# Optimization experiments

Measured on AMD Instinct MI355X. Metric: run time of the kernel, lower is better.

The kernel has to match this reference:

```python
import jax, jax.numpy as jnp
import numpy as np

EPS = 1e-8


def setup_inputs() -> dict:
    key = jax.random.key(0)
    k1, k2, k3 = jax.random.split(key, 3)
    B, K, L, D = 4, 64, 128, 768
    context = jax.random.normal(k1, (B, K, 2, L, D), dtype=jnp.float32)
    # MlpModule(input_size=D): Linear(D, D) -> ReLU -> Linear(D, 1)
    w1 = jax.random.normal(k2, (D, D), dtype=jnp.float32) * (1.0 / np.sqrt(D))
    b1 = jnp.zeros((D,), dtype=jnp.float32)
    w2 = jax.random.normal(k3, (D, 1), dtype=jnp.float32) * (1.0 / np.sqrt(D))
    b2 = jnp.zeros((1,), dtype=jnp.float32)
    return {"context": context, "w1": w1, "b1": b1, "w2": w2, "b2": b2}


def reference(context, w1, b1, w2, b2):
    # context: [B, K, 2, L, D]; slice 0 = context tokens, slice 1 = entity tokens
    ctx = context[:, :, 0, :, :]   # [B, K, L, D]
    ent = context[:, :, 1, :, :]   # [B, K, L, D]

    ctx_norm = jnp.linalg.norm(ctx, axis=-1, keepdims=True)  # [B, K, L, 1]
    ent_norm = jnp.linalg.norm(ent, axis=-1, keepdims=True)  # [B, K, L, 1]

    # cosine-similarity score matrix: [B, K, L, L]
    denom = ctx_norm * jnp.swapaxes(ent_norm, -1, -2) + EPS
    scores = jnp.einsum('bkld,bkmd->bklm', ctx, ent) / denom

    # normalized embeddings (torch code does in-place /= before the stack)
    ctx_n = ctx / ctx_norm
    ent_n = ent / ent_norm

    # top-1 match along entity axis, gather matched entity token per context token
    argmax_idx = jnp.argmax(scores, axis=-1)                       # [B, K, L] int
    matched = jnp.take_along_axis(ent_n, argmax_idx[..., None], axis=2)  # [B, K, L, D]

    pair = jnp.stack([ctx_n, matched], axis=-2)  # [B, K, L, 2, D]

    # MLP: Linear(D,D) -> ReLU -> Linear(D,1), then sum over the pair axis
    h = jax.nn.relu(jnp.einsum('bklpd,de->bklpe', pair, w1) + b1)
    out = jnp.einsum('bklpd,do->bklpo', h, w2) + b2   # [B, K, L, 2, 1]
    out = jnp.sum(out, axis=-2)                        # [B, K, L, 1]
    return jnp.squeeze(out, axis=-1)                   # [B, K, L]
```

## Files before the change

### kernel.cpp

```cpp
#include <hip/hip_runtime.h>
#include <hip/hip_bf16.h>
#include <stdint.h>

#define NB 4
#define NK 64
#define NL 128
#define ND 768
#define NBK (NB*NK)
#define NROW (NBK*NL)
#define LD2 (NL*ND)
#define EPSF 1e-8f

typedef __bf16 bf16x8 __attribute__((ext_vector_type(8)));
typedef float  f32x4  __attribute__((ext_vector_type(4)));

__device__ __forceinline__ int row_off(int r) {
  if (r < NROW) return r*ND + (r >> 7)*LD2;
  int r2 = r - NROW;
  return r2*ND + (r2 >> 7)*LD2 + LD2;
}

__global__ __launch_bounds__(256) void k0_w1t(const float* __restrict__ w1,
                                              __bf16* __restrict__ w1t) {
  __shared__ float tile[64][68];
  int kb = (blockIdx.x / 12) * 64, eb = (blockIdx.x % 12) * 64;
  int t = threadIdx.x;
  int r = t >> 2, c0 = (t & 3) * 16;
  #pragma unroll
  for (int j = 0; j < 4; j++) {
    f32x4 v = *(const f32x4*)(w1 + (kb + r)*ND + eb + c0 + j*4);
    *(f32x4*)&tile[r][c0 + j*4] = v;
  }
  __syncthreads();
  int e = t & 63, gi = t >> 6;
  int eg = eb + e;
  #pragma unroll
  for (int g2 = 0; g2 < 2; g2++) {
    int g = gi*2 + g2;
    bf16x8 o;
    #pragma unroll
    for (int j = 0; j < 8; j++) o[j] = (__bf16)tile[g*8 + j][e];
    int G = (kb >> 3) + (g ^ (eg & 7));
    *(bf16x8*)(w1t + eg*ND + G*8) = o;
  }
}

__global__ __launch_bounds__(256) void k2_scores(
    const float* __restrict__ ctxall, float* __restrict__ norm,
    int* __restrict__ amax) {
  __shared__ float at[2][16][68];
  __shared__ float bt[2][16][132];
  __shared__ float red[256];
  __shared__ float cnorm[64], enorm[128];
  int bk = blockIdx.x >> 1, half = blockIdx.x & 1;
  const float* cbase = ctxall + bk*2*LD2 + half*64*ND;
  const float* ebase = ctxall + bk*2*LD2 + LD2;
  int tid = threadIdx.x;
  int tr = tid >> 5, tc = tid & 31;
  int ar = tid >> 2, ak = (tid & 3)*4;
  int br = tid >> 1, bkk = (tid & 1)*8;

  float acc[8][4];
  #pragma unroll
  for (int j = 0; j < 8; j++)
    #pragma unroll
    for (int c = 0; c < 4; c++) acc[j][c] = 0.f;
  float sqa = 0.f, sqb = 0.f;

  f32x4 av  = *(const f32x4*)(cbase + ar*ND + ak);
  f32x4 bv0 = *(const f32x4*)(ebase + br*ND + bkk);
  f32x4 bv1 = *(const f32x4*)(ebase + br*ND + bkk + 4);

  int p = 0;
  for (int t = 0; t < 48; t++) {
    #pragma unroll
    for (int j = 0; j < 4; j++) { at[p][ak+j][ar] = av[j];     sqa += av[j]*av[j]; }
    #pragma unroll
    for (int j = 0; j < 4; j++) { bt[p][bkk+j][br] = bv0[j];   sqb += bv0[j]*bv0[j]; }
    #pragma unroll
    for (int j = 0; j < 4; j++) { bt[p][bkk+4+j][br] = bv1[j]; sqb += bv1[j]*bv1[j]; }
    __syncthreads();
    if (t < 47) {
      int k0 = (t+1)*16;
      av  = *(const f32x4*)(cbase + ar*ND + k0 + ak);
      bv0 = *(const f32x4*)(ebase + br*ND + k0 + bkk);
      bv1 = *(const f32x4*)(ebase + br*ND + k0 + bkk + 4);
    }
    #pragma unroll
    for (int kk = 0; kk < 16; kk++) {
      f32x4 a0 = *(const f32x4*)&at[p][kk][tr*8];
      f32x4 a1 = *(const f32x4*)&at[p][kk][tr*8 + 4];
      f32x4 b  = *(const f32x4*)&bt[p][kk][tc*4];
      #pragma unroll
      for (int j = 0; j < 4; j++)
        #pragma unroll
        for (int c = 0; c < 4; c++) {
          acc[j][c]   = fmaf(a0[j], b[c], acc[j][c]);
          acc[j+4][c] = fmaf(a1[j], b[c], acc[j+4][c]);
        }
    }
    p ^= 1;
  }

  red[tid] = sqa; __syncthreads();
  if (tid < 64) {
    float s = red[tid*4] + red[tid*4+1] + red[tid*4+2] + red[tid*4+3];
    float n = sqrtf(s);
    cnorm[tid] = n;
    norm[bk*NL + half*64 + tid] = n;
  }
  __syncthreads();
  red[tid] = sqb; __syncthreads();
  if (tid < 128) {
    float s = red[tid*2] + red[tid*2+1];
    float n = sqrtf(s);
    enorm[tid] = n;
    if (half == 0) norm[NROW + bk*NL + tid] = n;
  }
  __syncthreads();

  float en[4];
  #pragma unroll
  for (int c = 0; c < 4; c++) en[c] = enorm[tc*4 + c];

  float bestv[8]; int besti[8];
  #pragma unroll
  for (int j = 0; j < 8; j++) {
    float cn = cnorm[tr*8 + j];
    bestv[j] = -3.0e38f; besti[j] = 0;
    #pragma unroll
    for (int c = 0; c < 4; c++) {
      float s = acc[j][c] / (cn*en[c] + EPSF);
      if (s > bestv[j]) { bestv[j] = s; besti[j] = tc*4 + c; }
    }
  }
  #pragma unroll
  for (int off = 1; off < 32; off <<= 1) {
    #pragma unroll
    for (int j = 0; j < 8; j++) {
      float ov = __shfl_xor(bestv[j], off);
      int   oi = __shfl_xor(besti[j], off);
      if (ov > bestv[j] || (ov == bestv[j] && oi < besti[j])) { bestv[j] = ov; besti[j] = oi; }
    }
  }
  if (tc == 0) {
    #pragma unroll
    for (int j = 0; j < 8; j++) amax[bk*NL + half*64 + tr*8 + j] = besti[j];
  }
}

__global__ __launch_bounds__(256, 2) void k3_mlp(
    const float* __restrict__ ctxall, const float* __restrict__ norm,
    const __bf16* __restrict__ w1t, const float* __restrict__ b1,
    const float* __restrict__ w2, float* __restrict__ val) {
  __shared__ alignas(16) __bf16 btile[16*768];
  int tid = threadIdx.x;
  int wave = tid >> 6, lane = tid & 63;
  int quad = lane >> 4, eloc = lane & 15;
  int rbase = blockIdx.x*128 + wave*32;

  bf16x8 afrag[2][24];
  #pragma unroll
  for (int s = 0; s < 2; s++) {
    int r = rbase + s*16 + eloc;
    const float* src = ctxall + row_off(r);
    float rinv = 1.0f / norm[r];
    #pragma unroll
    for (int ks = 0; ks < 24; ks++) {
      const float* sp = src + ks*32 + quad*8;
      f32x4 v0 = *(const f32x4*)sp;
      f32x4 v1 = *(const f32x4*)(sp + 4);
      bf16x8 a;
      a[0] = (__bf16)(v0[0]*rinv); a[1] = (__bf16)(v0[1]*rinv);
      a[2] = (__bf16)(v0[2]*rinv); a[3] = (__bf16)(v0[3]*rinv);
      a[4] = (__bf16)(v1[0]*rinv); a[5] = (__bf16)(v1[1]*rinv);
      a[6] = (__bf16)(v1[2]*rinv); a[7] = (__bf16)(v1[3]*rinv);
      afrag[s][ks] = a;
    }
  }

  float oacc[2][4] = {{0,0,0,0},{0,0,0,0}};
  for (int nt = 0; nt < 48; nt++) {
    const __bf16* gsrc = w1t + nt*16*ND;
    __syncthreads();
    #pragma unroll
    for (int i = 0; i < 6; i++) {
      __builtin_amdgcn_global_load_lds(
        (const __attribute__((address_space(1))) unsigned int*)(gsrc + (i*256 + tid)*8),
        (__attribute__((address_space(3))) unsigned int*)(btile + (i*256 + tid)*8),
        16, 0, 0);
    }
    __syncthreads();

    f32x4 h0 = {0,0,0,0}, h1 = {0,0,0,0};
    #pragma unroll
    for (int ks = 0; ks < 24; ks++) {
      int g = ks*4 + quad;
      bf16x8 bfrag = *(const bf16x8*)(btile + eloc*ND + ((g ^ (eloc & 7))*8));
      h0 = __builtin_amdgcn_mfma_f32_16x16x32_bf16(afrag[0][ks], bfrag, h0, 0, 0, 0);
      h1 = __builtin_amdgcn_mfma_f32_16x16x32_bf16(afrag[1][ks], bfrag, h1, 0, 0, 0);
    }
    float b1v = b1[nt*16 + eloc];
    float w2v = w2[nt*16 + eloc];
    #pragma unroll
    for (int rr = 0; rr < 4; rr++) {
      oacc[0][rr] += fmaxf(h0[rr] + b1v, 0.f) * w2v;
      oacc[1][rr] += fmaxf(h1[rr] + b1v, 0.f) * w2v;
    }
  }
  #pragma unroll
  for (int m = 1; m < 16; m <<= 1)
    #pragma unroll
    for (int s = 0; s < 2; s++)
      #pragma unroll
      for (int rr = 0; rr < 4; rr++)
        oacc[s][rr] += __shfl_xor(oacc[s][rr], m);
  if (eloc == 0) {
    #pragma unroll
    for (int s = 0; s < 2; s++)
      #pragma unroll
      for (int rr = 0; rr < 4; rr++)
        val[rbase + s*16 + quad*4 + rr] = oacc[s][rr];
  }
}

__global__ void k4_out(const float* __restrict__ val, const int* __restrict__ amax,
                       const float* __restrict__ b2, float* __restrict__ out) {
  int i = blockIdx.x*256 + threadIdx.x;
  int bk = i >> 7;
  out[i] = val[i] + val[NROW + bk*NL + amax[i]] + 2.0f*b2[0];
}

extern "C" void kernel_launch(void* const* d_in, const int* in_sizes, int n_in,
                              void* d_out, int out_size, void* d_ws, size_t ws_size,
                              hipStream_t stream) {
  const float* ctxall = (const float*)d_in[0];
  const float* w1 = (const float*)d_in[1];
  const float* b1 = (const float*)d_in[2];
  const float* w2 = (const float*)d_in[3];
  const float* b2 = (const float*)d_in[4];
  float* out = (float*)d_out;

  char* ws = (char*)d_ws;
  float* norm = (float*)ws;
  int*   amax = (int*)(ws + 262144);
  float* val  = (float*)(ws + 262144 + 131072);
  __bf16* w1t = (__bf16*)(ws + 655360);

  hipLaunchKernelGGL(k0_w1t,   dim3(144),         dim3(256), 0, stream, w1, w1t);
  hipLaunchKernelGGL(k2_scores,dim3(2*NBK),       dim3(256), 0, stream, ctxall, norm, amax);
  hipLaunchKernelGGL(k3_mlp,   dim3(2*NROW/128),  dim3(256), 0, stream, ctxall, norm, w1t, b1, w2, val);
  hipLaunchKernelGGL(k4_out,   dim3(NROW/256),    dim3(256), 0, stream, val, amax, b2, out);
}
```

Before: 424.2 us.

## Screen argmax with split-bf16 MFMA, rescore near-ties in fp32, double-buffer W1 tiles

```diff
diff --git a/kernel.cpp b/kernel.cpp
--- a/kernel.cpp
+++ b/kernel.cpp
@@ -10,6 +10,8 @@
 #define NROW (NBK*NL)
 #define LD2 (NL*ND)
 #define EPSF 1e-8f
+#define THETA 2e-3f
+#define CAP 16384
 
 typedef __bf16 bf16x8 __attribute__((ext_vector_type(8)));
 typedef float  f32x4  __attribute__((ext_vector_type(4)));
@@ -21,8 +23,13 @@
 }
 
 __global__ __launch_bounds__(256) void k0_w1t(const float* __restrict__ w1,
-                                              __bf16* __restrict__ w1t) {
+                                              __bf16* __restrict__ w1t,
+                                              unsigned long long* __restrict__ amax2,
+                                              unsigned* __restrict__ cntg) {
   __shared__ float tile[64][68];
+  int idx = blockIdx.x*256 + threadIdx.x;
+  if (idx < NROW) amax2[idx] = 0ull;
+  if (idx == 0) *cntg = 0u;
   int kb = (blockIdx.x / 12) * 64, eb = (blockIdx.x % 12) * 64;
   int t = threadIdx.x;
   int r = t >> 2, c0 = (t & 3) * 16;
@@ -45,107 +52,146 @@
   }
 }
 
-__global__ __launch_bounds__(256) void k2_scores(
+__device__ __forceinline__ void cvt4(f32x4 v, unsigned& hp0, unsigned& hp1,
+                                     unsigned& lp0, unsigned& lp1, float& sq) {
+  unsigned u0 = __float_as_uint(v[0]), u1 = __float_as_uint(v[1]);
+  unsigned u2 = __float_as_uint(v[2]), u3 = __float_as_uint(v[3]);
+  hp0 = (u1 & 0xffff0000u) | (u0 >> 16);
+  hp1 = (u3 & 0xffff0000u) | (u2 >> 16);
+  float l0 = v[0] - __uint_as_float(u0 & 0xffff0000u);
+  float l1 = v[1] - __uint_as_float(u1 & 0xffff0000u);
+  float l2 = v[2] - __uint_as_float(u2 & 0xffff0000u);
+  float l3 = v[3] - __uint_as_float(u3 & 0xffff0000u);
+  lp0 = (__float_as_uint(l1) & 0xffff0000u) | (__float_as_uint(l0) >> 16);
+  lp1 = (__float_as_uint(l3) & 0xffff0000u) | (__float_as_uint(l2) >> 16);
+  sq += v[0]*v[0] + v[1]*v[1] + v[2]*v[2] + v[3]*v[3];
+}
+
+__global__ __launch_bounds__(512) void k2a_screen(
     const float* __restrict__ ctxall, float* __restrict__ norm,
-    int* __restrict__ amax) {
-  __shared__ float at[2][16][68];
-  __shared__ float bt[2][16][132];
-  __shared__ float red[256];
-  __shared__ float cnorm[64], enorm[128];
-  int bk = blockIdx.x >> 1, half = blockIdx.x & 1;
-  const float* cbase = ctxall + bk*2*LD2 + half*64*ND;
-  const float* ebase = ctxall + bk*2*LD2 + LD2;
-  int tid = threadIdx.x;
-  int tr = tid >> 5, tc = tid & 31;
-  int ar = tid >> 2, ak = (tid & 3)*4;
-  int br = tid >> 1, bkk = (tid & 1)*8;
-
-  float acc[8][4];
-  #pragma unroll
-  for (int j = 0; j < 8; j++)
-    #pragma unroll
-    for (int c = 0; c < 4; c++) acc[j][c] = 0.f;
-  float sqa = 0.f, sqb = 0.f;
-
-  f32x4 av  = *(const f32x4*)(cbase + ar*ND + ak);
-  f32x4 bv0 = *(const f32x4*)(ebase + br*ND + bkk);
-  f32x4 bv1 = *(const f32x4*)(ebase + br*ND + bkk + 4);
+    int* __restrict__ amax, unsigned* __restrict__ cntg,
+    unsigned* __restrict__ list) {
+  __shared__ alignas(16) __bf16 tiles[2][4][128*32];
+  __shared__ float einv_s[128];
+  int bk = blockIdx.x;
+  int t = threadIdx.x;
+  int mat = t >> 8, row = (t >> 1) & 127, kh = (t & 1) * 16;
+  const float* src = ctxall + bk*2*LD2 + mat*LD2 + row*ND + kh;
+  int w = t >> 6, lane = t & 63, quad = lane >> 4, eloc = lane & 15;
+
+  f32x4 pv[4];
+  #pragma unroll
+  for (int i = 0; i < 4; i++) pv[i] = *(const f32x4*)(src + i*4);
+  float sq = 0.f;
+  f32x4 acc[8];
+  #pragma unroll
+  for (int ct = 0; ct < 8; ct++) acc[ct] = (f32x4){0,0,0,0};
 
   int p = 0;
-  for (int t = 0; t < 48; t++) {
-    #pragma unroll
-    for (int j = 0; j < 4; j++) { at[p][ak+j][ar] = av[j];     sqa += av[j]*av[j]; }
-    #pragma unroll
-    for (int j = 0; j < 4; j++) { bt[p][bkk+j][br] = bv0[j];   sqb += bv0[j]*bv0[j]; }
-    #pragma unroll
-    for (int j = 0; j < 4; j++) { bt[p][bkk+4+j][br] = bv1[j]; sqb += bv1[j]*bv1[j]; }
+  for (int kt = 0; kt < 24; kt++) {
+    unsigned h0,h1,h2,h3, l0,l1,l2,l3;
+    cvt4(pv[0], h0, h1, l0, l1, sq);
+    cvt4(pv[1], h2, h3, l2, l3, sq);
+    __bf16* hdst = &tiles[p][2*mat  ][row*32 + kh];
+    __bf16* ldst = &tiles[p][2*mat+1][row*32 + kh];
+    *(uint4*)hdst = make_uint4(h0,h1,h2,h3);
+    *(uint4*)ldst = make_uint4(l0,l1,l2,l3);
+    cvt4(pv[2], h0, h1, l0, l1, sq);
+    cvt4(pv[3], h2, h3, l2, l3, sq);
+    *((uint4*)hdst + 1) = make_uint4(h0,h1,h2,h3);
+    *((uint4*)ldst + 1) = make_uint4(l0,l1,l2,l3);
     __syncthreads();
-    if (t < 47) {
-      int k0 = (t+1)*16;
-      av  = *(const f32x4*)(cbase + ar*ND + k0 + ak);
-      bv0 = *(const f32x4*)(ebase + br*ND + k0 + bkk);
-      bv1 = *(const f32x4*)(ebase + br*ND + k0 + bkk + 4);
-    }
-    #pragma unroll
-    for (int kk = 0; kk < 16; kk++) {
-      f32x4 a0 = *(const f32x4*)&at[p][kk][tr*8];
-      f32x4 a1 = *(const f32x4*)&at[p][kk][tr*8 + 4];
-      f32x4 b  = *(const f32x4*)&bt[p][kk][tc*4];
-      #pragma unroll
-      for (int j = 0; j < 4; j++)
-        #pragma unroll
-        for (int c = 0; c < 4; c++) {
-          acc[j][c]   = fmaf(a0[j], b[c], acc[j][c]);
-          acc[j+4][c] = fmaf(a1[j], b[c], acc[j+4][c]);
+    if (kt < 23) {
+      const float* s2 = src + (kt+1)*32;
+      #pragma unroll
+      for (int i = 0; i < 4; i++) pv[i] = *(const f32x4*)(s2 + i*4);
+    }
+    bf16x8 ah = *(const bf16x8*)&tiles[p][0][(w*16+eloc)*32 + quad*8];
+    bf16x8 al = *(const bf16x8*)&tiles[p][1][(w*16+eloc)*32 + quad*8];
+    #pragma unroll
+    for (int ct = 0; ct < 8; ct++) {
+      bf16x8 bh = *(const bf16x8*)&tiles[p][2][(ct*16+eloc)*32 + quad*8];
+      bf16x8 bl = *(const bf16x8*)&tiles[p][3][(ct*16+eloc)*32 + quad*8];
+      acc[ct] = __builtin_amdgcn_mfma_f32_16x16x32_bf16(al, bh, acc[ct], 0, 0, 0);
+      acc[ct] = __builtin_amdgcn_mfma_f32_16x16x32_bf16(ah, bl, acc[ct], 0, 0, 0);
+      acc[ct] = __builtin_amdgcn_mfma_f32_16x16x32_bf16(ah, bh, acc[ct], 0, 0, 0);
+    }
+    p ^= 1;
+  }
+
+  float stot = sq + __shfl_xor(sq, 1);
+  if ((t & 1) == 0) {
+    float n = sqrtf(stot);
+    if (mat == 0) norm[bk*NL + row] = n;
+    else { norm[NROW + bk*NL + row] = n; einv_s[row] = 1.0f / n; }
+  }
+  __syncthreads();
+
+  #pragma unroll
+  for (int rr = 0; rr < 4; rr++) {
+    float sc[8];
+    float best = -3.0e38f; int bcol = 0;
+    #pragma unroll
+    for (int ct = 0; ct < 8; ct++) {
+      sc[ct] = acc[ct][rr] * einv_s[ct*16 + eloc];
+      int col = ct*16 + eloc;
+      if (sc[ct] > best) { best = sc[ct]; bcol = col; }
+    }
+    #pragma unroll
+    for (int m = 1; m < 16; m <<= 1) {
+      float ov = __shfl_xor(best, m);
+      int   oc = __shfl_xor(bcol, m);
+      if (ov > best || (ov == best && oc < bcol)) { best = ov; bcol = oc; }
+    }
+    int grow = bk*NL + w*16 + quad*4 + rr;
+    if (eloc == 0) amax[grow] = bcol;
+    int cnt = 0;
+    #pragma unroll
+    for (int ct = 0; ct < 8; ct++) cnt += (sc[ct] >= best - THETA) ? 1 : 0;
+    #pragma unroll
+    for (int m = 1; m < 16; m <<= 1) cnt += __shfl_xor(cnt, m);
+    if (cnt >= 2) {
+      #pragma unroll
+      for (int ct = 0; ct < 8; ct++) {
+        if (sc[ct] >= best - THETA) {
+          unsigned idx = atomicAdd(cntg, 1u);
+          if (idx < CAP) list[idx] = ((unsigned)grow << 7) | (unsigned)(ct*16 + eloc);
         }
-    }
-    p ^= 1;
-  }
-
-  red[tid] = sqa; __syncthreads();
-  if (tid < 64) {
-    float s = red[tid*4] + red[tid*4+1] + red[tid*4+2] + red[tid*4+3];
-    float n = sqrtf(s);
-    cnorm[tid] = n;
-    norm[bk*NL + half*64 + tid] = n;
-  }
-  __syncthreads();
-  red[tid] = sqb; __syncthreads();
-  if (tid < 128) {
-    float s = red[tid*2] + red[tid*2+1];
-    float n = sqrtf(s);
-    enorm[tid] = n;
-    if (half == 0) norm[NROW + bk*NL + tid] = n;
-  }
-  __syncthreads();
-
-  float en[4];
-  #pragma unroll
-  for (int c = 0; c < 4; c++) en[c] = enorm[tc*4 + c];
-
-  float bestv[8]; int besti[8];
-  #pragma unroll
-  for (int j = 0; j < 8; j++) {
-    float cn = cnorm[tr*8 + j];
-    bestv[j] = -3.0e38f; besti[j] = 0;
-    #pragma unroll
-    for (int c = 0; c < 4; c++) {
-      float s = acc[j][c] / (cn*en[c] + EPSF);
-      if (s > bestv[j]) { bestv[j] = s; besti[j] = tc*4 + c; }
-    }
-  }
-  #pragma unroll
-  for (int off = 1; off < 32; off <<= 1) {
-    #pragma unroll
-    for (int j = 0; j < 8; j++) {
-      float ov = __shfl_xor(bestv[j], off);
-      int   oi = __shfl_xor(besti[j], off);
-      if (ov > bestv[j] || (ov == bestv[j] && oi < besti[j])) { bestv[j] = ov; besti[j] = oi; }
-    }
-  }
-  if (tc == 0) {
-    #pragma unroll
-    for (int j = 0; j < 8; j++) amax[bk*NL + half*64 + tr*8 + j] = besti[j];
+      }
+    }
+  }
+}
+
+__global__ __launch_bounds__(256) void k2b_rescore(
+    const float* __restrict__ ctxall, const float* __restrict__ norm,
+    const unsigned* __restrict__ cntg, const unsigned* __restrict__ list,
+    unsigned long long* __restrict__ amax2) {
+  unsigned n = *cntg; if (n > CAP) n = CAP;
+  int lane = threadIdx.x & 63;
+  unsigned wv = blockIdx.x*4 + (threadIdx.x >> 6);
+  for (unsigned e = wv; e < n; e += 256) {
+    unsigned ent = list[e];
+    int row = (int)(ent >> 7), col = (int)(ent & 127);
+    int bk = row >> 7;
+    const float* a = ctxall + row_off(row);
+    const float* b = ctxall + bk*2*LD2 + LD2 + col*ND;
+    float d = 0.f;
+    #pragma unroll
+    for (int i = 0; i < 3; i++) {
+      f32x4 va = *(const f32x4*)(a + lane*12 + i*4);
+      f32x4 vb = *(const f32x4*)(b + lane*12 + i*4);
+      d += va[0]*vb[0] + va[1]*vb[1] + va[2]*vb[2] + va[3]*vb[3];
+    }
+    #pragma unroll
+    for (int m = 1; m < 64; m <<= 1) d += __shfl_xor(d, m);
+    if (lane == 0) {
+      float cn = norm[row], en = norm[NROW + bk*NL + col];
+      float s = d / (cn*en + EPSF);
+      unsigned su = __float_as_uint(s);
+      unsigned ord = (su & 0x80000000u) ? ~su : (su | 0x80000000u);
+      unsigned long long key = ((unsigned long long)ord << 32) | (unsigned)(127 - col);
+      atomicMax(&amax2[row], key);
+    }
   }
 }
 
@@ -153,11 +199,19 @@
     const float* __restrict__ ctxall, const float* __restrict__ norm,
     const __bf16* __restrict__ w1t, const float* __restrict__ b1,
     const float* __restrict__ w2, float* __restrict__ val) {
-  __shared__ alignas(16) __bf16 btile[16*768];
+  __shared__ alignas(16) __bf16 btile[2][16*768];
   int tid = threadIdx.x;
   int wave = tid >> 6, lane = tid & 63;
   int quad = lane >> 4, eloc = lane & 15;
   int rbase = blockIdx.x*128 + wave*32;
+
+  #pragma unroll
+  for (int i = 0; i < 6; i++) {
+    __builtin_amdgcn_global_load_lds(
+      (const __attribute__((address_space(1))) unsigned int*)(w1t + (i*256 + tid)*8),
+      (__attribute__((address_space(3))) unsigned int*)(&btile[0][0] + (i*256 + tid)*8),
+      16, 0, 0);
+  }
 
   bf16x8 afrag[2][24];
   #pragma unroll
@@ -180,23 +234,24 @@
   }
 
   float oacc[2][4] = {{0,0,0,0},{0,0,0,0}};
+  int p = 0;
   for (int nt = 0; nt < 48; nt++) {
-    const __bf16* gsrc = w1t + nt*16*ND;
     __syncthreads();
-    #pragma unroll
-    for (int i = 0; i < 6; i++) {
-      __builtin_amdgcn_global_load_lds(
-        (const __attribute__((address_space(1))) unsigned int*)(gsrc + (i*256 + tid)*8),
-        (__attribute__((address_space(3))) unsigned int*)(btile + (i*256 + tid)*8),
-        16, 0, 0);
-    }
-    __syncthreads();
-
+    if (nt < 47) {
+      const __bf16* gsrc = w1t + (nt+1)*16*ND;
+      #pragma unroll
+      for (int i = 0; i < 6; i++) {
+        __builtin_amdgcn_global_load_lds(
+          (const __attribute__((address_space(1))) unsigned int*)(gsrc + (i*256 + tid)*8),
+          (__attribute__((address_space(3))) unsigned int*)(&btile[p^1][0] + (i*256 + tid)*8),
+          16, 0, 0);
+      }
+    }
     f32x4 h0 = {0,0,0,0}, h1 = {0,0,0,0};
     #pragma unroll
     for (int ks = 0; ks < 24; ks++) {
       int g = ks*4 + quad;
-      bf16x8 bfrag = *(const bf16x8*)(btile + eloc*ND + ((g ^ (eloc & 7))*8));
+      bf16x8 bfrag = *(const bf16x8*)(&btile[p][0] + eloc*ND + ((g ^ (eloc & 7))*8));
       h0 = __builtin_amdgcn_mfma_f32_16x16x32_bf16(afrag[0][ks], bfrag, h0, 0, 0, 0);
       h1 = __builtin_amdgcn_mfma_f32_16x16x32_bf16(afrag[1][ks], bfrag, h1, 0, 0, 0);
     }
@@ -207,6 +262,7 @@
       oacc[0][rr] += fmaxf(h0[rr] + b1v, 0.f) * w2v;
       oacc[1][rr] += fmaxf(h1[rr] + b1v, 0.f) * w2v;
     }
+    p ^= 1;
   }
   #pragma unroll
   for (int m = 1; m < 16; m <<= 1)
@@ -225,10 +281,13 @@
 }
 
 __global__ void k4_out(const float* __restrict__ val, const int* __restrict__ amax,
+                       const unsigned long long* __restrict__ amax2,
                        const float* __restrict__ b2, float* __restrict__ out) {
   int i = blockIdx.x*256 + threadIdx.x;
   int bk = i >> 7;
-  out[i] = val[i] + val[NROW + bk*NL + amax[i]] + 2.0f*b2[0];
+  unsigned long long k = amax2[i];
+  int a = k ? (127 - (int)(k & 127ull)) : amax[i];
+  out[i] = val[i] + val[NROW + bk*NL + a] + 2.0f*b2[0];
 }
 
 extern "C" void kernel_launch(void* const* d_in, const int* in_sizes, int n_in,
@@ -242,13 +301,17 @@
   float* out = (float*)d_out;
 
   char* ws = (char*)d_ws;
-  float* norm = (float*)ws;
-  int*   amax = (int*)(ws + 262144);
-  float* val  = (float*)(ws + 262144 + 131072);
-  __bf16* w1t = (__bf16*)(ws + 655360);
-
-  hipLaunchKernelGGL(k0_w1t,   dim3(144),         dim3(256), 0, stream, w1, w1t);
-  hipLaunchKernelGGL(k2_scores,dim3(2*NBK),       dim3(256), 0, stream, ctxall, norm, amax);
-  hipLaunchKernelGGL(k3_mlp,   dim3(2*NROW/128),  dim3(256), 0, stream, ctxall, norm, w1t, b1, w2, val);
-  hipLaunchKernelGGL(k4_out,   dim3(NROW/256),    dim3(256), 0, stream, val, amax, b2, out);
-}
+  float*    norm = (float*)ws;
+  int*      amax = (int*)(ws + 262144);
+  float*    val  = (float*)(ws + 393216);
+  __bf16*   w1t  = (__bf16*)(ws + 655360);
+  unsigned long long* amax2 = (unsigned long long*)(ws + 1835008);
+  unsigned* cntg = (unsigned*)(ws + 2097152);
+  unsigned* list = (unsigned*)(ws + 2097156);
+
+  hipLaunchKernelGGL(k0_w1t,     dim3(144),        dim3(256), 0, stream, w1, w1t, amax2, cntg);
+  hipLaunchKernelGGL(k2a_screen, dim3(NBK),        dim3(512), 0, stream, ctxall, norm, amax, cntg, list);
+  hipLaunchKernelGGL(k2b_rescore,dim3(64),         dim3(256), 0, stream, ctxall, norm, cntg, list, amax2);
+  hipLaunchKernelGGL(k3_mlp,     dim3(2*NROW/128), dim3(256), 0, stream, ctxall, norm, w1t, b1, w2, val);
+  hipLaunchKernelGGL(k4_out,     dim3(NROW/256),   dim3(256), 0, stream, val, amax, amax2, b2, out);
+}
```

Result: faster. 395.8 us (-6.7%).
